# Kernel tuning notes

Measured on AMD Instinct MI355X. Metric: run time of the kernel, lower is better.

The kernel has to match this reference:

```python
import jax, jax.numpy as jnp
import numpy as np

B = 1024        # sessions
N = 32          # nodes per session
S = 50          # steps per session
H = 256         # hidden_size
V = 50000       # vocab size of embedding_table
GROUP = 3       # items pooled per step (reshape(-1, 3, H) in source)
SAN_BLOCKS = 3


def setup_inputs() -> dict:
    key = jax.random.key(0)
    ks = jax.random.split(key, 16)
    node_embedding = jax.random.normal(ks[0], (B * N, H), jnp.float32)
    emb_weight = jax.random.normal(ks[1], (V, H), jnp.float32) * 0.02
    batch = jnp.repeat(jnp.arange(B, dtype=jnp.int32), N)           # session id per node
    sequence = jax.random.randint(ks[2], (B * S, GROUP), 0, N + 1)  # local idx; ==N -> zero pad row
    itemset_len = jax.random.randint(ks[3], (B * S,), 1, GROUP + 1).astype(jnp.float32)
    sequence_len = jnp.full((B,), S, dtype=jnp.int32)               # steps per session
    cue = jax.random.randint(ks[4], (B,), 0, V)
    sc = 1.0 / np.sqrt(H)
    in_proj_w = jax.random.normal(ks[5], (3 * H, H), jnp.float32) * sc
    in_proj_b = jnp.zeros((3 * H,), jnp.float32)
    out_proj_w = jax.random.normal(ks[6], (H, H), jnp.float32) * sc
    out_proj_b = jnp.zeros((H,), jnp.float32)
    d1_w = jax.random.normal(ks[7], (H, H), jnp.float32) * sc
    d1_b = jnp.zeros((H,), jnp.float32)
    d2_w = jax.random.normal(ks[8], (H, H), jnp.float32) * sc
    d2_b = jnp.zeros((H,), jnp.float32)
    W3_w = jax.random.normal(ks[9], (H, 2 * H), jnp.float32) * (1.0 / np.sqrt(2 * H))
    W3_b = jnp.zeros((H,), jnp.float32)
    return {
        "node_embedding": node_embedding, "emb_weight": emb_weight,
        "itemset_len": itemset_len, "in_proj_w": in_proj_w, "in_proj_b": in_proj_b,
        "out_proj_w": out_proj_w, "out_proj_b": out_proj_b,
        "d1_w": d1_w, "d1_b": d1_b, "d2_w": d2_w, "d2_b": d2_b,
        "W3_w": W3_w, "W3_b": W3_b,
        "batch": batch, "sequence": sequence, "sequence_len": sequence_len, "cue": cue,
    }


def reference(node_embedding, emb_weight, itemset_len, in_proj_w, in_proj_b,
              out_proj_w, out_proj_b, d1_w, d1_b, d2_w, d2_b, W3_w, W3_b,
              batch, sequence, sequence_len, cue):
    # Eval mode: dropout disabled.
    total_nodes, h = node_embedding.shape
    nsess = sequence_len.shape[0]
    total_steps = sequence.shape[0]

    # Per-session node counts and exclusive offsets (replaces torch.split on ragged batch).
    sections = jnp.bincount(batch, length=nsess)
    offsets = jnp.cumsum(sections) - sections

    # Append one global zero row; local index == sections[sess] maps to it
    # (matches the per-session zero row in v_i_zeros).
    nodes_pad = jnp.concatenate([node_embedding, jnp.zeros((1, h), node_embedding.dtype)], axis=0)
    step_sess = jnp.repeat(jnp.arange(nsess), sequence_len, total_repeat_length=total_steps)
    sec_s = sections[step_sess][:, None]
    off_s = offsets[step_sess][:, None]
    gidx = jnp.where(sequence == sec_s, total_nodes, off_s + sequence)  # [T, 3] global indices

    # session_i: 3-way sum of gathered node embeddings / itemset_len  -> [T, H]
    step_emb = nodes_pad[gidx].sum(axis=1) / itemset_len[:, None]

    # Last step of each session (both v_n and the position s_g is read from).
    last_idx = jnp.cumsum(sequence_len) - 1
    v_n = step_emb[last_idx]  # [B, H]

    # nn.MultiheadAttention receives (L=1, N=steps, E=H): softmax over a single key
    # is identically 1, so MHA == out_proj(v_proj(x)) applied per step independently.
    # Hence the SAN chain on the last step equals the chain applied to v_n alone.
    Wv = in_proj_w[2 * h:]
    bv = in_proj_b[2 * h:]
    x = v_n
    for _ in range(SAN_BLOCKS):
        attn = (x @ Wv.T + bv) @ out_proj_w.T + out_proj_b
        # Residual FFN (dropout off in eval): x + d2(relu(d1(x)))
        x = attn + (jax.nn.relu(attn @ d1_w.T + d1_b) @ d2_w.T + d2_b)
    s_g = x  # [B, H]

    s_h = jnp.concatenate([v_n, s_g], axis=1) @ W3_w.T + W3_b  # [B, H]
    y_hat = jnp.sum(s_h * emb_weight[cue], axis=1)             # [B]
    all_scores = s_h @ emb_weight.T                            # [B, V]
    return y_hat, all_scores
```

## Files before the change

kernel.cpp:

```cpp
#include <hip/hip_runtime.h>
#include <hip/hip_bf16.h>
#include <stdint.h>

typedef __attribute__((ext_vector_type(8))) short short8;
typedef __attribute__((ext_vector_type(4))) float f32x4;

#define HD 256

__device__ __forceinline__ ushort f2bf(float f) {
  union { float f; uint32_t u; } x; x.f = f;
  uint32_t r = (x.u + 0x7fffu + ((x.u >> 16) & 1u)) >> 16;
  return (ushort)r;
}

__device__ __forceinline__ int swz(int row, int col) {
  int chunk = (col >> 3) ^ (row & 7);
  return row * 256 + chunk * 8 + (col & 7);
}

__global__ void prep1_kernel(const int* __restrict__ batch, int total_nodes,
                             int* __restrict__ sections,
                             const float* __restrict__ in_proj_w,
                             const float* __restrict__ out_proj_w,
                             const float* __restrict__ d1_w,
                             const float* __restrict__ d2_w,
                             const float* __restrict__ W3_w,
                             ushort* __restrict__ Wv_bf, ushort* __restrict__ Po_bf,
                             ushort* __restrict__ d1_bf, ushort* __restrict__ d2_bf,
                             ushort* __restrict__ W3_bf) {
  int stride = gridDim.x * blockDim.x;
  int t0 = blockIdx.x * blockDim.x + threadIdx.x;
  for (int i = t0; i < total_nodes; i += stride)
    atomicAdd(&sections[batch[i]], 1);
  for (int i = t0; i < HD * HD; i += stride) {
    Wv_bf[i] = f2bf(in_proj_w[2 * HD * HD + i]);
    Po_bf[i] = f2bf(out_proj_w[i]);
    d1_bf[i] = f2bf(d1_w[i]);
    d2_bf[i] = f2bf(d2_w[i]);
  }
  for (int i = t0; i < HD * 2 * HD; i += stride)
    W3_bf[i] = f2bf(W3_w[i]);
}

__global__ void scan_kernel(const int* __restrict__ seq_len, int* __restrict__ sections,
                            int* __restrict__ offsets, int* __restrict__ last_idx,
                            int nsess) {
  __shared__ int s1[1024];
  __shared__ int s2[1024];
  int t = threadIdx.x;
  int v1 = (t < nsess) ? sections[t] : 0;
  int v2 = (t < nsess) ? seq_len[t] : 0;
  s1[t] = v1; s2[t] = v2;
  for (int d = 1; d < 1024; d <<= 1) {
    __syncthreads();
    int a1 = (t >= d) ? s1[t - d] : 0;
    int a2 = (t >= d) ? s2[t - d] : 0;
    __syncthreads();
    s1[t] += a1; s2[t] += a2;
  }
  __syncthreads();
  if (t < nsess) {
    offsets[t] = s1[t] - v1;
    last_idx[t] = s2[t] - 1;
  }
}

template<bool RELU, bool RESID, bool WACC>
__device__ __forceinline__ void gemm_stage(const ushort* inA, const ushort* __restrict__ Wbf,
                                           const float* __restrict__ bias,
                                           float* accf, ushort* outB) {
  int t = threadIdx.x;
  int lane = t & 63, wid = t >> 6;
  int la = lane & 15, g = lane >> 4;
  int colb = wid * 64;
  f32x4 acc[4] = {{0.f,0.f,0.f,0.f},{0.f,0.f,0.f,0.f},{0.f,0.f,0.f,0.f},{0.f,0.f,0.f,0.f}};
#pragma unroll
  for (int kk = 0; kk < 8; ++kk) {
    short8 a = *(const short8*)&inA[swz(la, kk * 32 + g * 8)];
#pragma unroll
    for (int ct = 0; ct < 4; ++ct) {
      int col = colb + ct * 16 + la;
      short8 b = *(const short8*)&Wbf[col * HD + kk * 32 + g * 8];
      acc[ct] = __builtin_amdgcn_mfma_f32_16x16x32_bf16(a, b, acc[ct], 0, 0, 0);
    }
  }
#pragma unroll
  for (int ct = 0; ct < 4; ++ct) {
    int col = colb + ct * 16 + la;
    float bia = bias[col];
#pragma unroll
    for (int r = 0; r < 4; ++r) {
      int ro = g * 4 + r;
      float v = acc[ct][r] + bia;
      if (RELU) v = fmaxf(v, 0.f);
      if (RESID) v += accf[ro * HD + col];
      if (WACC) accf[ro * HD + col] = v;
      outB[swz(ro, col)] = f2bf(v);
    }
  }
}

__device__ __forceinline__ void stage_fence() {
  __syncthreads();
  __builtin_amdgcn_sched_barrier(0);
}

__global__ __launch_bounds__(256) void sh_kernel(
    const float* __restrict__ node_emb, const float* __restrict__ emb_w,
    const float* __restrict__ itemset_len, const float* __restrict__ in_proj_b,
    const float* __restrict__ out_proj_b, const float* __restrict__ d1_b,
    const float* __restrict__ d2_b, const float* __restrict__ W3_b,
    const int* __restrict__ sequence, const int* __restrict__ cue,
    const int* __restrict__ sections, const int* __restrict__ offsets,
    const int* __restrict__ last_idx,
    const ushort* __restrict__ Wv_bf, const ushort* __restrict__ Po_bf,
    const ushort* __restrict__ d1_bf, const ushort* __restrict__ d2_bf,
    const ushort* __restrict__ W3_bf,
    ushort* __restrict__ sh_bf, float* __restrict__ y_hat, int group) {
  __shared__ float accf[16 * HD];
  __shared__ ushort vn_bf[16 * HD];
  __shared__ ushort bufA[16 * HD];
  __shared__ ushort bufB[16 * HD];
  __shared__ float red[16][17];
  int t = threadIdx.x;
  int b0 = blockIdx.x * 16;

  {
    int r = t >> 4, cg = t & 15;
    int sess = b0 + r;
    int li = last_idx[sess];
    float inv = 1.0f / itemset_len[li];
    int sec = sections[sess], off = offsets[sess];
    float4 s0 = {0,0,0,0}, s1 = {0,0,0,0}, s2 = {0,0,0,0}, s3 = {0,0,0,0};
    for (int gi = 0; gi < group; ++gi) {
      int sq = sequence[li * group + gi];
      if (sq == sec) continue;
      const float4* src = (const float4*)(node_emb + (size_t)(off + sq) * HD + cg * 16);
      float4 v;
      v = src[0]; s0.x += v.x; s0.y += v.y; s0.z += v.z; s0.w += v.w;
      v = src[1]; s1.x += v.x; s1.y += v.y; s1.z += v.z; s1.w += v.w;
      v = src[2]; s2.x += v.x; s2.y += v.y; s2.z += v.z; s2.w += v.w;
      v = src[3]; s3.x += v.x; s3.y += v.y; s3.z += v.z; s3.w += v.w;
    }
    float v[16];
    v[0]=s0.x; v[1]=s0.y; v[2]=s0.z; v[3]=s0.w;
    v[4]=s1.x; v[5]=s1.y; v[6]=s1.z; v[7]=s1.w;
    v[8]=s2.x; v[9]=s2.y; v[10]=s2.z; v[11]=s2.w;
    v[12]=s3.x; v[13]=s3.y; v[14]=s3.z; v[15]=s3.w;
#pragma unroll
    for (int j = 0; j < 16; ++j)
      vn_bf[swz(r, cg * 16 + j)] = f2bf(v[j] * inv);
  }
  stage_fence();

  const ushort* cur = vn_bf;
#pragma unroll 1
  for (int sb = 0; sb < 3; ++sb) {
    gemm_stage<false, false, false>(cur, Wv_bf, in_proj_b + 2 * HD, nullptr, bufA);
    stage_fence();
    gemm_stage<false, false, true>(bufA, Po_bf, out_proj_b, accf, bufB);
    stage_fence();
    gemm_stage<true, false, false>(bufB, d1_bf, d1_b, nullptr, bufA);
    stage_fence();
    gemm_stage<false, true, false>(bufA, d2_bf, d2_b, accf, bufB);
    stage_fence();
    cur = bufB;
  }

  {
    int lane = t & 63, wid = t >> 6;
    int la = lane & 15, g = lane >> 4;
    int colb = wid * 64;
    f32x4 acc[4] = {{0.f,0.f,0.f,0.f},{0.f,0.f,0.f,0.f},{0.f,0.f,0.f,0.f},{0.f,0.f,0.f,0.f}};
#pragma unroll
    for (int kk = 0; kk < 16; ++kk) {
      const ushort* src = (kk < 8) ? vn_bf : cur;
      short8 a = *(const short8*)&src[swz(la, (kk & 7) * 32 + g * 8)];
#pragma unroll
      for (int ct = 0; ct < 4; ++ct) {
        int col = colb + ct * 16 + la;
        short8 b = *(const short8*)&W3_bf[col * 2 * HD + kk * 32 + g * 8];
        acc[ct] = __builtin_amdgcn_mfma_f32_16x16x32_bf16(a, b, acc[ct], 0, 0, 0);
      }
    }
#pragma unroll
    for (int ct = 0; ct < 4; ++ct) {
      int col = colb + ct * 16 + la;
      float bia = W3_b[col];
#pragma unroll
      for (int r = 0; r < 4; ++r) {
        int ro = g * 4 + r;
        float v = acc[ct][r] + bia;
        accf[ro * HD + col] = v;
        sh_bf[(size_t)(b0 + ro) * HD + col] = f2bf(v);
      }
    }
  }
  stage_fence();

  {
    int r = t >> 4, cg = t & 15;
    const float* er = emb_w + (size_t)cue[b0 + r] * HD + cg * 16;
    float p = 0.f;
#pragma unroll
    for (int j = 0; j < 16; ++j) p += accf[r * HD + cg * 16 + j] * er[j];
    red[r][cg] = p;
    __syncthreads();
    if (cg == 0) {
      float s = 0.f;
#pragma unroll
      for (int k = 0; k < 16; ++k) s += red[r][k];
      y_hat[b0 + r] = s;
    }
  }
}

__global__ __launch_bounds__(256) void score_kernel(
    const ushort* __restrict__ sh_bf, const float* __restrict__ emb_w,
    float* __restrict__ scores, int nrows, int V) {
  __shared__ ushort ebuf[64 * HD];
  int t = threadIdx.x;
  int c0 = blockIdx.x * 64;
#pragma unroll
  for (int i = 0; i < 8; ++i) {
    int c = t + i * 256;
    int row = c >> 5, q = c & 31;
    if (c0 + row < V) {
      const float4* src = (const float4*)(emb_w + (size_t)(c0 + row) * HD + q * 8);
      float4 v0 = src[0], v1 = src[1];
      short8 u;
      u[0] = (short)f2bf(v0.x); u[1] = (short)f2bf(v0.y);
      u[2] = (short)f2bf(v0.z); u[3] = (short)f2bf(v0.w);
      u[4] = (short)f2bf(v1.x); u[5] = (short)f2bf(v1.y);
      u[6] = (short)f2bf(v1.z); u[7] = (short)f2bf(v1.w);
      *(short8*)&ebuf[row * 256 + ((q ^ (row & 7)) * 8)] = u;
    }
  }
  __syncthreads();

  int lane = t & 63, wid = t >> 6;
  int la = lane & 15, g = lane >> 4;
  int nrb = nrows >> 6;
  for (int rb = 0; rb < nrb; ++rb) {
    int r0 = rb * 64 + wid * 16;
    const ushort* arow = sh_bf + (size_t)(r0 + la) * HD;
    short8 a[8];
#pragma unroll
    for (int kk = 0; kk < 8; ++kk) a[kk] = *(const short8*)&arow[kk * 32 + g * 8];
    f32x4 acc[4] = {{0.f,0.f,0.f,0.f},{0.f,0.f,0.f,0.f},{0.f,0.f,0.f,0.f},{0.f,0.f,0.f,0.f}};
#pragma unroll
    for (int kk = 0; kk < 8; ++kk) {
#pragma unroll
      for (int ct = 0; ct < 4; ++ct) {
        int brow = ct * 16 + la;
        short8 b = *(const short8*)&ebuf[brow * 256 + (((kk * 4 + g) ^ (brow & 7)) * 8)];
        acc[ct] = __builtin_amdgcn_mfma_f32_16x16x32_bf16(a[kk], b, acc[ct], 0, 0, 0);
      }
    }
#pragma unroll
    for (int ct = 0; ct < 4; ++ct) {
      int col = c0 + ct * 16 + la;
      if (col < V) {
#pragma unroll
        for (int r = 0; r < 4; ++r) {
          int m = r0 + g * 4 + r;
          scores[(size_t)m * V + col] = acc[ct][r];
        }
      }
    }
  }
}

extern "C" void kernel_launch(void* const* d_in, const int* in_sizes, int n_in,
                              void* d_out, int out_size, void* d_ws, size_t ws_size,
                              hipStream_t stream) {
  const float* node_emb   = (const float*)d_in[0];
  const float* emb_w      = (const float*)d_in[1];
  const float* itemset_len= (const float*)d_in[2];
  const float* in_proj_w  = (const float*)d_in[3];
  const float* in_proj_b  = (const float*)d_in[4];
  const float* out_proj_w = (const float*)d_in[5];
  const float* out_proj_b = (const float*)d_in[6];
  const float* d1_w       = (const float*)d_in[7];
  const float* d1_b       = (const float*)d_in[8];
  const float* d2_w       = (const float*)d_in[9];
  const float* d2_b       = (const float*)d_in[10];
  const float* W3_w       = (const float*)d_in[11];
  const float* W3_b       = (const float*)d_in[12];
  const int*   batch      = (const int*)d_in[13];
  const int*   sequence   = (const int*)d_in[14];
  const int*   seq_len    = (const int*)d_in[15];
  const int*   cue        = (const int*)d_in[16];

  int total_nodes = in_sizes[0] / HD;
  int V           = in_sizes[1] / HD;
  int nsess       = in_sizes[15];
  int total_steps = in_sizes[2];
  int group       = in_sizes[14] / total_steps;

  char* ws = (char*)d_ws;
  int* sections   = (int*)(ws);
  int* offsets    = (int*)(ws + 4096);
  int* last_idx   = (int*)(ws + 8192);
  ushort* sh_bf   = (ushort*)(ws + 16384);
  ushort* Wv_bf   = (ushort*)(ws + 16384 + 524288);
  ushort* Po_bf   = Wv_bf + HD * HD;
  ushort* d1_bf   = Po_bf + HD * HD;
  ushort* d2_bf   = d1_bf + HD * HD;
  ushort* W3_bf   = d2_bf + HD * HD;

  float* y_hat  = (float*)d_out;
  float* scores = (float*)d_out + nsess;

  hipMemsetAsync(sections, 0, (size_t)nsess * sizeof(int), stream);
  prep1_kernel<<<512, 256, 0, stream>>>(batch, total_nodes, sections,
                                        in_proj_w, out_proj_w, d1_w, d2_w, W3_w,
                                        Wv_bf, Po_bf, d1_bf, d2_bf, W3_bf);
  scan_kernel<<<1, 1024, 0, stream>>>(seq_len, sections, offsets, last_idx, nsess);
  sh_kernel<<<nsess / 16, 256, 0, stream>>>(node_emb, emb_w, itemset_len, in_proj_b,
                                            out_proj_b, d1_b, d2_b, W3_b,
                                            sequence, cue, sections, offsets, last_idx,
                                            Wv_bf, Po_bf, d1_bf, d2_bf, W3_bf,
                                            sh_bf, y_hat, group);
  score_kernel<<<(V + 63) / 64, 256, 0, stream>>>(sh_bf, emb_w, scores, nsess, V);
}
```

Baseline: 164.9 us.

## Widen sh_kernel to 1024 threads with one 16-column MFMA tile per wave

The SAN/W3 chain kernel now runs 16 waves per block instead of 4, so each wave computes a single 16x16 output tile per GEMM stage instead of four. The gather and the cue dot product are remapped to 64 threads per session row, and the dot product uses a wave shuffle reduction instead of a shared-memory reduction. The aim is to cut per-wave serial MFMA chains and latency in this small-grid (64-block) kernel. In exchange, each B-load has less reuse per wave and barriers now synchronise more waves.

New measurement: 162.8 us. No clear change (-1.3%).

```diff
diff --git a/kernel.cpp b/kernel.cpp
--- a/kernel.cpp
+++ b/kernel.cpp
@@ -3,6 +3,7 @@
 #include <stdint.h>
 
 typedef __attribute__((ext_vector_type(8))) short short8;
+typedef __attribute__((ext_vector_type(4))) short short4v;
 typedef __attribute__((ext_vector_type(4))) float f32x4;
 
 #define HD 256
@@ -66,37 +67,29 @@
 }
 
 template<bool RELU, bool RESID, bool WACC>
-__device__ __forceinline__ void gemm_stage(const ushort* inA, const ushort* __restrict__ Wbf,
-                                           const float* __restrict__ bias,
-                                           float* accf, ushort* outB) {
+__device__ __forceinline__ void gemm_stage16(const ushort* inA, const ushort* __restrict__ Wbf,
+                                             const float* __restrict__ bias,
+                                             float* accf, ushort* outB) {
   int t = threadIdx.x;
   int lane = t & 63, wid = t >> 6;
   int la = lane & 15, g = lane >> 4;
-  int colb = wid * 64;
-  f32x4 acc[4] = {{0.f,0.f,0.f,0.f},{0.f,0.f,0.f,0.f},{0.f,0.f,0.f,0.f},{0.f,0.f,0.f,0.f}};
+  int col = wid * 16 + la;
+  f32x4 acc = {0.f, 0.f, 0.f, 0.f};
 #pragma unroll
   for (int kk = 0; kk < 8; ++kk) {
     short8 a = *(const short8*)&inA[swz(la, kk * 32 + g * 8)];
-#pragma unroll
-    for (int ct = 0; ct < 4; ++ct) {
-      int col = colb + ct * 16 + la;
-      short8 b = *(const short8*)&Wbf[col * HD + kk * 32 + g * 8];
-      acc[ct] = __builtin_amdgcn_mfma_f32_16x16x32_bf16(a, b, acc[ct], 0, 0, 0);
-    }
-  }
-#pragma unroll
-  for (int ct = 0; ct < 4; ++ct) {
-    int col = colb + ct * 16 + la;
-    float bia = bias[col];
-#pragma unroll
-    for (int r = 0; r < 4; ++r) {
-      int ro = g * 4 + r;
-      float v = acc[ct][r] + bia;
-      if (RELU) v = fmaxf(v, 0.f);
-      if (RESID) v += accf[ro * HD + col];
-      if (WACC) accf[ro * HD + col] = v;
-      outB[swz(ro, col)] = f2bf(v);
-    }
+    short8 b = *(const short8*)&Wbf[col * HD + kk * 32 + g * 8];
+    acc = __builtin_amdgcn_mfma_f32_16x16x32_bf16(a, b, acc, 0, 0, 0);
+  }
+  float bia = bias[col];
+#pragma unroll
+  for (int r = 0; r < 4; ++r) {
+    int ro = g * 4 + r;
+    float v = acc[r] + bia;
+    if (RELU) v = fmaxf(v, 0.f);
+    if (RESID) v += accf[ro * HD + col];
+    if (WACC) accf[ro * HD + col] = v;
+    outB[swz(ro, col)] = f2bf(v);
   }
 }
 
@@ -105,7 +98,7 @@
   __builtin_amdgcn_sched_barrier(0);
 }
 
-__global__ __launch_bounds__(256) void sh_kernel(
+__global__ __launch_bounds__(1024, 1) void sh_kernel(
     const float* __restrict__ node_emb, const float* __restrict__ emb_w,
     const float* __restrict__ itemset_len, const float* __restrict__ in_proj_b,
     const float* __restrict__ out_proj_b, const float* __restrict__ d1_b,
@@ -121,48 +114,39 @@
   __shared__ ushort vn_bf[16 * HD];
   __shared__ ushort bufA[16 * HD];
   __shared__ ushort bufB[16 * HD];
-  __shared__ float red[16][17];
   int t = threadIdx.x;
   int b0 = blockIdx.x * 16;
 
   {
-    int r = t >> 4, cg = t & 15;
+    int r = t >> 6, cg = t & 63;
     int sess = b0 + r;
     int li = last_idx[sess];
     float inv = 1.0f / itemset_len[li];
     int sec = sections[sess], off = offsets[sess];
-    float4 s0 = {0,0,0,0}, s1 = {0,0,0,0}, s2 = {0,0,0,0}, s3 = {0,0,0,0};
+    float4 s = {0.f, 0.f, 0.f, 0.f};
     for (int gi = 0; gi < group; ++gi) {
       int sq = sequence[li * group + gi];
       if (sq == sec) continue;
-      const float4* src = (const float4*)(node_emb + (size_t)(off + sq) * HD + cg * 16);
-      float4 v;
-      v = src[0]; s0.x += v.x; s0.y += v.y; s0.z += v.z; s0.w += v.w;
-      v = src[1]; s1.x += v.x; s1.y += v.y; s1.z += v.z; s1.w += v.w;
-      v = src[2]; s2.x += v.x; s2.y += v.y; s2.z += v.z; s2.w += v.w;
-      v = src[3]; s3.x += v.x; s3.y += v.y; s3.z += v.z; s3.w += v.w;
-    }
-    float v[16];
-    v[0]=s0.x; v[1]=s0.y; v[2]=s0.z; v[3]=s0.w;
-    v[4]=s1.x; v[5]=s1.y; v[6]=s1.z; v[7]=s1.w;
-    v[8]=s2.x; v[9]=s2.y; v[10]=s2.z; v[11]=s2.w;
-    v[12]=s3.x; v[13]=s3.y; v[14]=s3.z; v[15]=s3.w;
-#pragma unroll
-    for (int j = 0; j < 16; ++j)
-      vn_bf[swz(r, cg * 16 + j)] = f2bf(v[j] * inv);
+      float4 v = *(const float4*)(node_emb + (size_t)(off + sq) * HD + cg * 4);
+      s.x += v.x; s.y += v.y; s.z += v.z; s.w += v.w;
+    }
+    short4v u;
+    u[0] = (short)f2bf(s.x * inv); u[1] = (short)f2bf(s.y * inv);
+    u[2] = (short)f2bf(s.z * inv); u[3] = (short)f2bf(s.w * inv);
+    *(short4v*)&vn_bf[swz(r, cg * 4)] = u;
   }
   stage_fence();
 
   const ushort* cur = vn_bf;
 #pragma unroll 1
   for (int sb = 0; sb < 3; ++sb) {
-    gemm_stage<false, false, false>(cur, Wv_bf, in_proj_b + 2 * HD, nullptr, bufA);
-    stage_fence();
-    gemm_stage<false, false, true>(bufA, Po_bf, out_proj_b, accf, bufB);
-    stage_fence();
-    gemm_stage<true, false, false>(bufB, d1_bf, d1_b, nullptr, bufA);
-    stage_fence();
-    gemm_stage<false, true, false>(bufA, d2_bf, d2_b, accf, bufB);
+    gemm_stage16<false, false, false>(cur, Wv_bf, in_proj_b + 2 * HD, nullptr, bufA);
+    stage_fence();
+    gemm_stage16<false, false, true>(bufA, Po_bf, out_proj_b, accf, bufB);
+    stage_fence();
+    gemm_stage16<true, false, false>(bufB, d1_bf, d1_b, nullptr, bufA);
+    stage_fence();
+    gemm_stage16<false, true, false>(bufA, d2_bf, d2_b, accf, bufB);
     stage_fence();
     cur = bufB;
   }
@@ -170,48 +154,34 @@
   {
     int lane = t & 63, wid = t >> 6;
     int la = lane & 15, g = lane >> 4;
-    int colb = wid * 64;
-    f32x4 acc[4] = {{0.f,0.f,0.f,0.f},{0.f,0.f,0.f,0.f},{0.f,0.f,0.f,0.f},{0.f,0.f,0.f,0.f}};
+    int col = wid * 16 + la;
+    f32x4 acc = {0.f, 0.f, 0.f, 0.f};
 #pragma unroll
     for (int kk = 0; kk < 16; ++kk) {
       const ushort* src = (kk < 8) ? vn_bf : cur;
       short8 a = *(const short8*)&src[swz(la, (kk & 7) * 32 + g * 8)];
-#pragma unroll
-      for (int ct = 0; ct < 4; ++ct) {
-        int col = colb + ct * 16 + la;
-        short8 b = *(const short8*)&W3_bf[col * 2 * HD + kk * 32 + g * 8];
-        acc[ct] = __builtin_amdgcn_mfma_f32_16x16x32_bf16(a, b, acc[ct], 0, 0, 0);
-      }
-    }
-#pragma unroll
-    for (int ct = 0; ct < 4; ++ct) {
-      int col = colb + ct * 16 + la;
-      float bia = W3_b[col];
-#pragma unroll
-      for (int r = 0; r < 4; ++r) {
-        int ro = g * 4 + r;
-        float v = acc[ct][r] + bia;
-        accf[ro * HD + col] = v;
-        sh_bf[(size_t)(b0 + ro) * HD + col] = f2bf(v);
-      }
+      short8 b = *(const short8*)&W3_bf[col * 2 * HD + kk * 32 + g * 8];
+      acc = __builtin_amdgcn_mfma_f32_16x16x32_bf16(a, b, acc, 0, 0, 0);
+    }
+    float bia = W3_b[col];
+#pragma unroll
+    for (int r = 0; r < 4; ++r) {
+      int ro = g * 4 + r;
+      float v = acc[r] + bia;
+      accf[ro * HD + col] = v;
+      sh_bf[(size_t)(b0 + ro) * HD + col] = f2bf(v);
     }
   }
   stage_fence();
 
   {
-    int r = t >> 4, cg = t & 15;
-    const float* er = emb_w + (size_t)cue[b0 + r] * HD + cg * 16;
-    float p = 0.f;
-#pragma unroll
-    for (int j = 0; j < 16; ++j) p += accf[r * HD + cg * 16 + j] * er[j];
-    red[r][cg] = p;
-    __syncthreads();
-    if (cg == 0) {
-      float s = 0.f;
-#pragma unroll
-      for (int k = 0; k < 16; ++k) s += red[r][k];
-      y_hat[b0 + r] = s;
-    }
+    int r = t >> 6, lane = t & 63;
+    const float4 er = *(const float4*)(emb_w + (size_t)cue[b0 + r] * HD + lane * 4);
+    const float* ar = &accf[r * HD + lane * 4];
+    float p = ar[0] * er.x + ar[1] * er.y + ar[2] * er.z + ar[3] * er.w;
+#pragma unroll
+    for (int off = 32; off >= 1; off >>= 1) p += __shfl_down(p, off, 64);
+    if (lane == 0) y_hat[b0 + r] = p;
   }
 }
 
@@ -317,10 +287,10 @@
                                         in_proj_w, out_proj_w, d1_w, d2_w, W3_w,
                                         Wv_bf, Po_bf, d1_bf, d2_bf, W3_bf);
   scan_kernel<<<1, 1024, 0, stream>>>(seq_len, sections, offsets, last_idx, nsess);
-  sh_kernel<<<nsess / 16, 256, 0, stream>>>(node_emb, emb_w, itemset_len, in_proj_b,
-                                            out_proj_b, d1_b, d2_b, W3_b,
-                                            sequence, cue, sections, offsets, last_idx,
-                                            Wv_bf, Po_bf, d1_bf, d2_bf, W3_bf,
-                                            sh_bf, y_hat, group);
+  sh_kernel<<<nsess / 16, 1024, 0, stream>>>(node_emb, emb_w, itemset_len, in_proj_b,
+                                             out_proj_b, d1_b, d2_b, W3_b,
+                                             sequence, cue, sections, offsets, last_idx,
+                                             Wv_bf, Po_bf, d1_bf, d2_bf, W3_bf,
+                                             sh_bf, y_hat, group);
   score_kernel<<<(V + 63) / 64, 256, 0, stream>>>(sh_bf, emb_w, scores, nsess, V);
 }
```
